# Performance work log

Hardware: AMD Instinct MI355X
Metric: run time of the kernel (lower is better)

Reference implementation:

```python
import jax, jax.numpy as jnp
import numpy as np

HIDDEN = 1152
HEADS = 16
HEAD_DIM = HIDDEN // HEADS  # 72
SCALE = HEAD_DIM ** -0.5


def setup_inputs() -> dict:
    key = jax.random.key(0)
    ks = jax.random.split(key, 9)
    B, S = 16, 729
    init = lambda k, shape: jax.random.normal(k, shape, dtype=jnp.float32) * (shape[0] ** -0.5)
    return {
        "hidden_states": jax.random.normal(ks[0], (B, S, HIDDEN), dtype=jnp.float32),
        "Wq": init(ks[1], (HIDDEN, HIDDEN)), "bq": jnp.zeros((HIDDEN,), jnp.float32),
        "Wk": init(ks[2], (HIDDEN, HIDDEN)), "bk": jnp.zeros((HIDDEN,), jnp.float32),
        "Wv": init(ks[3], (HIDDEN, HIDDEN)), "bv": jnp.zeros((HIDDEN,), jnp.float32),
        "Wo": init(ks[4], (HIDDEN, HIDDEN)), "bo": jnp.zeros((HIDDEN,), jnp.float32),
    }


def reference(hidden_states, Wq, bq, Wk, bk, Wv, bv, Wo, bo):
    B, S, D = hidden_states.shape
    # QKV projections, split heads: [B, S, H, Dh]
    q = (hidden_states @ Wq + bq).reshape(B, S, HEADS, HEAD_DIM)
    k = (hidden_states @ Wk + bk).reshape(B, S, HEADS, HEAD_DIM)
    v = (hidden_states @ Wv + bv).reshape(B, S, HEADS, HEAD_DIM)
    # Scores: [B, H, S, S]
    scores = jnp.einsum("bqhd,bkhd->bhqk", q, k) * jnp.asarray(SCALE, q.dtype)
    # Softmax computed in float32 (as in the original layer), cast back
    attn = jax.nn.softmax(scores.astype(jnp.float32), axis=-1).astype(q.dtype)
    # Weighted values: [B, S, H, Dh] -> [B, S, D]
    out = jnp.einsum("bhqk,bkhd->bqhd", attn, v).reshape(B, S, D)
    return out @ Wo + bo
```

## Files before the change

kernel.cpp:

```cpp
#include <hip/hip_runtime.h>
#include <hip/hip_bf16.h>

#define HD    1152
#define NHD   16
#define DH    72
#define DHP   80
#define NB    16
#define SEQ   729
#define SP    736
#define MTOT  (NB*SEQ)
#define MPAD  11776
#define VROWS 96
#define QSCALE (0.117851130197757930f * 1.4426950408889634f)

typedef __attribute__((ext_vector_type(8))) short short8;
typedef __attribute__((ext_vector_type(4))) float f32x4;
typedef __attribute__((ext_vector_type(16))) float f32x16;
typedef __attribute__((ext_vector_type(4))) unsigned u32x4;
typedef unsigned short us;

__device__ __forceinline__ us f2bf(float x){
  unsigned u = __float_as_uint(x);
  u += 0x7FFFu + ((u >> 16) & 1u);
  return (us)(u >> 16);
}

__device__ __forceinline__ unsigned cvtpk_bf16(float lo, float hi){
  unsigned r;
  asm("v_cvt_pk_bf16_f32 %0, %1, %2" : "=v"(r) : "v"(lo), "v"(hi));
  return r;
}

#define GLD16(g, s) __builtin_amdgcn_global_load_lds( \
    (const __attribute__((address_space(1))) void*)(g), \
    (__attribute__((address_space(3))) void*)(s), 16, 0, 0)

#define OFF_HSB   ((size_t)0)
#define OFF_WQKV  ((size_t)27131904)
#define OFF_WO    ((size_t)35094528)
#define OFF_Q     ((size_t)37748736)
#define OFF_K     ((size_t)67608576)
#define OFF_V     ((size_t)97755136)
#define WS_END    ((size_t)133931008)

#define CVT_BLOCKS 13122
__global__ void prep_kernel(const float* __restrict__ hs, us* __restrict__ hsb,
                            const float* __restrict__ Wq, const float* __restrict__ Wk,
                            const float* __restrict__ Wv, const float* __restrict__ Wo,
                            us* __restrict__ wqkvT, us* __restrict__ woT){
  __shared__ float t[32][33];
  const int b = blockIdx.x, tid = threadIdx.x;
  if (b < CVT_BLOCKS){
    int i = b*256 + tid;
    float4 v = ((const float4*)hs)[i];
    ushort4 o;
    o.x = f2bf(v.x); o.y = f2bf(v.y); o.z = f2bf(v.z); o.w = f2bf(v.w);
    ((ushort4*)hsb)[i] = o;
    return;
  }
  const int bb = b - CVT_BLOCKS;
  const int sel = bb / 1296, cell = bb % 1296;
  const int k0 = (cell/36)*32, n0 = (cell%36)*32;
  const float* W = (sel==0)?Wq:(sel==1)?Wk:(sel==2)?Wv:Wo;
  us* outT = (sel<3) ? (wqkvT + (size_t)sel*HD*HD) : woT;
  const int tx = tid & 31, ty = tid >> 5;
  #pragma unroll
  for (int j=0;j<32;j+=8) t[ty+j][tx] = W[(size_t)(k0+ty+j)*HD + n0 + tx];
  __syncthreads();
  #pragma unroll
  for (int j=0;j<32;j+=8) outT[(size_t)(n0+ty+j)*HD + k0 + tx] = f2bf(t[tx][ty+j]);
}

template<int MODE>
__global__ __launch_bounds__(512, 4) void gemm_kernel(
    const us* __restrict__ A, const us* __restrict__ BT,
    const float* __restrict__ bias_q, const float* __restrict__ bias_k,
    const float* __restrict__ bias_v,
    float* __restrict__ outF,
    us* __restrict__ Qp, us* __restrict__ Kp, us* __restrict__ Vt)
{
  constexpr int TILES_N = (MODE==1) ? 27 : 9;
  constexpr int NPHYS   = (MPAD/128)*TILES_N/2;
  constexpr int NT = HD/32;

  int p;
  {
    int orig = blockIdx.x;
    constexpr int q = NPHYS >> 3, r = NPHYS & 7;
    int xcd = orig & 7, idx = orig >> 3;
    p = (xcd < r ? xcd*(q+1) : r*(q+1) + (xcd-r)*q) + idx;
  }
  const int tid = threadIdx.x, w = tid>>6, l = tid&63;
  const int g  = w>>2;
  const int wl = w&3;
  const int lr = l&15, lg = l>>4;
  const int wm = wl>>1, wn = wl&1;

  const int tile = p*2 + g;
  const int tn = tile % TILES_N, tm = tile / TILES_N;

  __shared__ __align__(16) us As[2][2][4096];
  __shared__ __align__(16) us Bs[2][2][4096];

  const int srow = wl*32 + (l>>2);
  const int scol = (l&3)*8;
  const us* gA = A  + (size_t)(tm*128 + srow)*HD + scol;
  const us* gB = BT + (size_t)(tn*128 + srow)*HD + scol;

#define STAGEP(kb, buf) do { \
    GLD16(gA + (kb),          &As[g][buf][wl*1024]); \
    GLD16(gA + (kb) + 16*HD,  &As[g][buf][wl*1024 + 512]); \
    GLD16(gB + (kb),          &Bs[g][buf][wl*1024]); \
    GLD16(gB + (kb) + 16*HD,  &Bs[g][buf][wl*1024 + 512]); \
  } while(0)

  f32x4 acc[4][4];
  #pragma unroll
  for (int i=0;i<4;i++)
    #pragma unroll
    for (int j=0;j<4;j++) acc[i][j] = (f32x4){0.f,0.f,0.f,0.f};

  STAGEP(0, 0);
  STAGEP(32, 1);

  for (int kt = 0; kt < NT-1; kt++){
    const int cur = kt & 1;
    asm volatile("s_waitcnt vmcnt(4)" ::: "memory");
    __builtin_amdgcn_sched_barrier(0);
    __builtin_amdgcn_s_barrier();
    __builtin_amdgcn_sched_barrier(0);

    short8 af[4], bfr[4];
    #pragma unroll
    for (int mi=0;mi<4;mi++) af[mi]  = *(const short8*)(&As[g][cur][(wm*64 + mi*16 + lr)*32 + lg*8]);
    #pragma unroll
    for (int ni=0;ni<4;ni++) bfr[ni] = *(const short8*)(&Bs[g][cur][(wn*64 + ni*16 + lr)*32 + lg*8]);

    asm volatile("s_waitcnt lgkmcnt(0)" ::: "memory");
    __builtin_amdgcn_sched_barrier(0);
    __builtin_amdgcn_s_barrier();
    __builtin_amdgcn_sched_barrier(0);

    if (kt + 2 < NT) STAGEP((kt+2)*32, cur);

    __builtin_amdgcn_s_setprio(1);
    #pragma unroll
    for (int mi=0;mi<4;mi++)
      #pragma unroll
      for (int ni=0;ni<4;ni++)
        acc[mi][ni] = __builtin_amdgcn_mfma_f32_16x16x32_bf16(af[mi], bfr[ni], acc[mi][ni], 0, 0, 0);
    __builtin_amdgcn_s_setprio(0);
  }
  {
    constexpr int cur = (NT-1) & 1;
    asm volatile("s_waitcnt vmcnt(0)" ::: "memory");
    __builtin_amdgcn_sched_barrier(0);
    __builtin_amdgcn_s_barrier();
    __builtin_amdgcn_sched_barrier(0);
    short8 af[4], bfr[4];
    #pragma unroll
    for (int mi=0;mi<4;mi++) af[mi]  = *(const short8*)(&As[g][cur][(wm*64 + mi*16 + lr)*32 + lg*8]);
    #pragma unroll
    for (int ni=0;ni<4;ni++) bfr[ni] = *(const short8*)(&Bs[g][cur][(wn*64 + ni*16 + lr)*32 + lg*8]);
    #pragma unroll
    for (int mi=0;mi<4;mi++)
      #pragma unroll
      for (int ni=0;ni<4;ni++)
        acc[mi][ni] = __builtin_amdgcn_mfma_f32_16x16x32_bf16(af[mi], bfr[ni], acc[mi][ni], 0, 0, 0);
  }
#undef STAGEP

  if (MODE == 0){
    #pragma unroll
    for (int mi=0;mi<4;mi++){
      #pragma unroll
      for (int j=0;j<4;j++){
        int m = tm*128 + wm*64 + mi*16 + lg*4 + j;
        if (m < MTOT){
          #pragma unroll
          for (int ni=0;ni<4;ni++){
            int n = tn*128 + wn*64 + ni*16 + lr;
            outF[(size_t)m*HD + n] = acc[mi][ni][j] + bias_q[n];
          }
        }
      }
    }
  } else {
    asm volatile("s_waitcnt lgkmcnt(0)" ::: "memory");
    __builtin_amdgcn_sched_barrier(0);
    __builtin_amdgcn_s_barrier();
    __builtin_amdgcn_sched_barrier(0);

    if (tn >= 18){
      float* scr = (float*)(&As[0][0][0]) + w*(16*17);
      #pragma unroll
      for (int mi=0;mi<4;mi++){
        int m = tm*128 + wm*64 + mi*16 + lr;
        int b = m / SEQ;
        int s = m - b*SEQ;
        bool ok = (m < MTOT);
        #pragma unroll
        for (int ni=0;ni<4;ni++){
          #pragma unroll
          for (int j=0;j<4;j++) scr[(lg*4+j)*17 + lr] = acc[mi][ni][j];
          asm volatile("s_waitcnt lgkmcnt(0)" ::: "memory");
          float tv[4];
          #pragma unroll
          for (int j=0;j<4;j++) tv[j] = scr[lr*17 + lg*4 + j];
          asm volatile("s_waitcnt lgkmcnt(0)" ::: "memory");
          if (ok){
            #pragma unroll
            for (int j=0;j<4;j++){
              int n = tn*128 + wn*64 + ni*16 + lg*4 + j;
              int c = n - 2*HD;
              int h = c / DH;
              int d = c - h*DH;
              int bh = b*NHD + h;
              Vt[(size_t)bh*(VROWS*SP) + (size_t)d*SP + s] = f2bf(tv[j] + bias_v[c]);
            }
          }
        }
      }
    } else {
      const bool isQ = (tn < 9);
      const int nbase = isQ ? 0 : HD;
      const float* bias = isQ ? bias_q : bias_k;
      #pragma unroll
      for (int mi=0;mi<4;mi++){
        #pragma unroll
        for (int j=0;j<4;j++){
          int m = tm*128 + wm*64 + mi*16 + lg*4 + j;
          if (m >= MTOT) continue;
          int b = m / SEQ;
          int s = m - b*SEQ;
          #pragma unroll
          for (int ni=0;ni<4;ni++){
            int n = tn*128 + wn*64 + ni*16 + lr;
            int c = n - nbase;
            int h = c / DH;
            int d = c - h*DH;
            int bh = b*NHD + h;
            float v = acc[mi][ni][j] + bias[c];
            if (isQ){
              Qp[(size_t)bh*(SEQ*DHP) + (size_t)s*DHP + d] = f2bf(v*QSCALE);
              if (d < 8)
                Qp[(size_t)bh*(SEQ*DHP) + (size_t)s*DHP + 72 + d] = 0;
            } else {
              Kp[(size_t)bh*(SP*DHP) + (size_t)s*DHP + d] = f2bf(v);
            }
          }
        }
      }
    }
  }
}

__device__ __forceinline__ void pv_subtile(const f32x16 s, const us* __restrict__ vcol,
                                           int hi, f32x16 (&o)[3]){
  unsigned A[4], B[4], xA[4], xB[4];
  #pragma unroll
  for (int g=0; g<4; g++){
    A[g]  = cvtpk_bf16(s[4*g+0], s[4*g+1]);
    B[g]  = cvtpk_bf16(s[4*g+2], s[4*g+3]);
    xA[g] = (unsigned)__shfl_xor((int)A[g], 32);
    xB[g] = (unsigned)__shfl_xor((int)B[g], 32);
  }
  __builtin_amdgcn_s_setprio(1);
  #pragma unroll
  for (int ks=0; ks<2; ks++){
    unsigned w0 = hi ? xA[2*ks+1] : A[2*ks];
    unsigned w1 = hi ? xB[2*ks+1] : B[2*ks];
    unsigned w2 = hi ? A[2*ks+1]  : xA[2*ks];
    unsigned w3 = hi ? B[2*ks+1]  : xB[2*ks];
    u32x4 pw = {w0, w1, w2, w3};
    short8 pa = __builtin_bit_cast(short8, pw);
    #pragma unroll
    for (int dt=0; dt<3; dt++){
      short8 vf = *(const short8*)(vcol + (size_t)(dt*32)*SP + ks*16 + hi*8);
      o[dt] = __builtin_amdgcn_mfma_f32_32x32x16_bf16(pa, vf, o[dt], 0, 0, 0);
    }
  }
  __builtin_amdgcn_s_setprio(0);
}

__global__ __launch_bounds__(256) void attn_kernel(
    const us* __restrict__ Qp, const us* __restrict__ Kp,
    const us* __restrict__ Vt, us* __restrict__ ctx)
{
  const int blk = blockIdx.x;
  const int xcd = blk & 7, ii = blk >> 3;
  const int bh  = xcd*32 + ii/6;
  const int qt6 = ii % 6;
  const int tid = threadIdx.x, w = tid>>6, l = tid&63;
  const int lane = l & 31, hi = l >> 5;

  const int qbase = (qt6*4 + w)*32;
  if (qbase >= SEQ) return;

  const us* Qb = Qp + (size_t)bh*(SEQ*DHP);
  const us* Kb = Kp + (size_t)bh*(SP*DHP);
  const us* Vb = Vt + (size_t)bh*(VROWS*SP);

  int qr = qbase + lane; if (qr > SEQ-1) qr = SEQ-1;
  short8 qf[5];
  #pragma unroll
  for (int c=0;c<5;c++) qf[c] = *(const short8*)(Qb + (size_t)qr*DHP + c*16 + hi*8);

  f32x16 o[3];
  #pragma unroll
  for (int dt=0; dt<3; dt++)
    #pragma unroll
    for (int r=0;r<16;r++) o[dt][r] = 0.f;

  float m = -1e30f, lsum = 0.f;

  for (int kt=0; kt<12; kt++){
    const int kb = kt*64;
    f32x16 s0, s1;
    #pragma unroll
    for (int r=0;r<16;r++){ s0[r]=0.f; s1[r]=0.f; }

    const us* krow0 = Kb + (size_t)(kb + lane)*DHP + hi*8;
    __builtin_amdgcn_s_setprio(1);
    #pragma unroll
    for (int c=0;c<5;c++){
      short8 kf = *(const short8*)(krow0 + c*16);
      s0 = __builtin_amdgcn_mfma_f32_32x32x16_bf16(kf, qf[c], s0, 0, 0, 0);
    }
    __builtin_amdgcn_s_setprio(0);
    if (kt < 11){
      const us* krow1 = krow0 + 32*DHP;
      __builtin_amdgcn_s_setprio(1);
      #pragma unroll
      for (int c=0;c<5;c++){
        short8 kf = *(const short8*)(krow1 + c*16);
        s1 = __builtin_amdgcn_mfma_f32_32x32x16_bf16(kf, qf[c], s1, 0, 0, 0);
      }
      __builtin_amdgcn_s_setprio(0);
    } else {
      #pragma unroll
      for (int r=0;r<16;r++){
        const int base = 704 + (r&3) + 8*(r>>2);
        s0[r] = (base + 4*hi >= SEQ) ? -1e30f : s0[r];
        s1[r] = -1e30f;
      }
    }

    float tmax = -1e30f;
    #pragma unroll
    for (int r=0;r<16;r++) tmax = fmaxf(tmax, fmaxf(s0[r], s1[r]));
    tmax = fmaxf(tmax, __shfl_xor(tmax, 32));

    if (!__all(tmax <= m + 8.0f)){
      float mn = fmaxf(m, tmax);
      float sc = exp2f(m - mn);
      m = mn;
      lsum *= sc;
      #pragma unroll
      for (int dt=0; dt<3; dt++)
        #pragma unroll
        for (int r=0;r<16;r++) o[dt][r] *= sc;
    }

    float su = 0.f;
    #pragma unroll
    for (int r=0;r<16;r++){ float pp = exp2f(s0[r]-m); s0[r]=pp; su += pp; }
    #pragma unroll
    for (int r=0;r<16;r++){ float pp = exp2f(s1[r]-m); s1[r]=pp; su += pp; }
    su += __shfl_xor(su, 32);
    lsum += su;

    const us* vcol = Vb + (size_t)lane*SP + kb;
    pv_subtile(s0, vcol, hi, o);
    if (kt < 11) pv_subtile(s1, vcol + 32, hi, o);
  }

  float linv = 1.0f / lsum;
  const int b = bh >> 4, h = bh & 15;
  #pragma unroll
  for (int r=0;r<16;r++){
    const int qloc = (r&3) + 8*(r>>2) + 4*hi;
    float lv = __shfl(linv, qloc);
    int q = qbase + qloc;
    if (q < SEQ){
      us* crow = ctx + ((size_t)(b*SEQ + q))*HD + h*DH;
      #pragma unroll
      for (int dt=0; dt<3; dt++){
        int d = dt*32 + lane;
        if (d < DH) crow[d] = f2bf(o[dt][r] * lv);
      }
    }
  }
}

extern "C" void kernel_launch(void* const* d_in, const int* in_sizes, int n_in,
                              void* d_out, int out_size, void* d_ws, size_t ws_size,
                              hipStream_t stream) {
  const float* hs = (const float*)d_in[0];
  const float* Wq = (const float*)d_in[1]; const float* bq = (const float*)d_in[2];
  const float* Wk = (const float*)d_in[3]; const float* bk = (const float*)d_in[4];
  const float* Wv = (const float*)d_in[5]; const float* bv = (const float*)d_in[6];
  const float* Wo = (const float*)d_in[7]; const float* bo = (const float*)d_in[8];
  float* out = (float*)d_out;
  char* ws = (char*)d_ws;
  if (ws_size < WS_END) return;

  us* hsb   = (us*)(ws + OFF_HSB);
  us* wqkvT = (us*)(ws + OFF_WQKV);
  us* woT   = (us*)(ws + OFF_WO);
  us* Qp    = (us*)(ws + OFF_Q);
  us* Kp    = (us*)(ws + OFF_K);
  us* Vt    = (us*)(ws + OFF_V);
  us* ctx   = hsb;

  prep_kernel<<<CVT_BLOCKS + 4*1296, 256, 0, stream>>>(hs, hsb, Wq, Wk, Wv, Wo,
                                                       wqkvT, woT);

  gemm_kernel<1><<<(MPAD/128)*27/2, 512, 0, stream>>>(hsb, wqkvT, bq, bk, bv,
                                                      nullptr, Qp, Kp, Vt);

  attn_kernel<<<1536, 256, 0, stream>>>(Qp, Kp, Vt, ctx);

  gemm_kernel<0><<<(MPAD/128)*9/2, 512, 0, stream>>>(ctx, woT, bo, nullptr, nullptr,
                                                     out, nullptr, nullptr, nullptr);
}
```

Measured before the change: 345.9 us.

## Process two 32-row query subtiles per wave to reuse K/V loads

Each wave in the attention kernel now handles 64 query rows as two 32-row subtiles, and blocks shrink from 256 to 128 threads. K and V fragment addresses are shared across both subtiles, so each loaded K/V tile feeds twice as much MFMA work. The online softmax state is duplicated per subtile. This roughly doubles accumulator and Q-fragment register use, which may lower occupancy. Query tiles past SEQ are no longer skipped early and are handled by clamping rows and masking the stores.

```diff
diff --git a/kernel.cpp b/kernel.cpp
--- a/kernel.cpp
+++ b/kernel.cpp
@@ -283,7 +283,7 @@
   __builtin_amdgcn_s_setprio(0);
 }
 
-__global__ __launch_bounds__(256) void attn_kernel(
+__global__ __launch_bounds__(128) void attn_kernel(
     const us* __restrict__ Qp, const us* __restrict__ Kp,
     const us* __restrict__ Vt, us* __restrict__ ctx)
 {
@@ -294,100 +294,111 @@
   const int tid = threadIdx.x, w = tid>>6, l = tid&63;
   const int lane = l & 31, hi = l >> 5;
 
-  const int qbase = (qt6*4 + w)*32;
-  if (qbase >= SEQ) return;
+  const int qbase = (qt6*2 + w)*64;
 
   const us* Qb = Qp + (size_t)bh*(SEQ*DHP);
   const us* Kb = Kp + (size_t)bh*(SP*DHP);
   const us* Vb = Vt + (size_t)bh*(VROWS*SP);
 
-  int qr = qbase + lane; if (qr > SEQ-1) qr = SEQ-1;
-  short8 qf[5];
-  #pragma unroll
-  for (int c=0;c<5;c++) qf[c] = *(const short8*)(Qb + (size_t)qr*DHP + c*16 + hi*8);
-
-  f32x16 o[3];
-  #pragma unroll
-  for (int dt=0; dt<3; dt++)
-    #pragma unroll
-    for (int r=0;r<16;r++) o[dt][r] = 0.f;
-
-  float m = -1e30f, lsum = 0.f;
+  short8 qf[2][5];
+  #pragma unroll
+  for (int st=0; st<2; st++){
+    int qr = qbase + st*32 + lane; if (qr > SEQ-1) qr = SEQ-1;
+    #pragma unroll
+    for (int c=0;c<5;c++) qf[st][c] = *(const short8*)(Qb + (size_t)qr*DHP + c*16 + hi*8);
+  }
+
+  f32x16 o[2][3];
+  #pragma unroll
+  for (int st=0; st<2; st++)
+    #pragma unroll
+    for (int dt=0; dt<3; dt++)
+      #pragma unroll
+      for (int r=0;r<16;r++) o[st][dt][r] = 0.f;
+
+  float m[2] = {-1e30f,-1e30f}, lsum[2] = {0.f,0.f};
 
   for (int kt=0; kt<12; kt++){
     const int kb = kt*64;
-    f32x16 s0, s1;
-    #pragma unroll
-    for (int r=0;r<16;r++){ s0[r]=0.f; s1[r]=0.f; }
-
     const us* krow0 = Kb + (size_t)(kb + lane)*DHP + hi*8;
-    __builtin_amdgcn_s_setprio(1);
-    #pragma unroll
-    for (int c=0;c<5;c++){
-      short8 kf = *(const short8*)(krow0 + c*16);
-      s0 = __builtin_amdgcn_mfma_f32_32x32x16_bf16(kf, qf[c], s0, 0, 0, 0);
+    const us* vcol  = Vb + (size_t)lane*SP + kb;
+
+    #pragma unroll
+    for (int st=0; st<2; st++){
+      f32x16 s0, s1;
+      #pragma unroll
+      for (int r=0;r<16;r++){ s0[r]=0.f; s1[r]=0.f; }
+
+      __builtin_amdgcn_s_setprio(1);
+      #pragma unroll
+      for (int c=0;c<5;c++){
+        short8 kf = *(const short8*)(krow0 + c*16);
+        s0 = __builtin_amdgcn_mfma_f32_32x32x16_bf16(kf, qf[st][c], s0, 0, 0, 0);
+      }
+      __builtin_amdgcn_s_setprio(0);
+      if (kt < 11){
+        const us* krow1 = krow0 + 32*DHP;
+        __builtin_amdgcn_s_setprio(1);
+        #pragma unroll
+        for (int c=0;c<5;c++){
+          short8 kf = *(const short8*)(krow1 + c*16);
+          s1 = __builtin_amdgcn_mfma_f32_32x32x16_bf16(kf, qf[st][c], s1, 0, 0, 0);
+        }
+        __builtin_amdgcn_s_setprio(0);
+      } else {
+        #pragma unroll
+        for (int r=0;r<16;r++){
+          const int base = 704 + (r&3) + 8*(r>>2);
+          s0[r] = (base + 4*hi >= SEQ) ? -1e30f : s0[r];
+          s1[r] = -1e30f;
+        }
+      }
+
+      float tmax = -1e30f;
+      #pragma unroll
+      for (int r=0;r<16;r++) tmax = fmaxf(tmax, fmaxf(s0[r], s1[r]));
+      tmax = fmaxf(tmax, __shfl_xor(tmax, 32));
+
+      if (!__all(tmax <= m[st] + 8.0f)){
+        float mn = fmaxf(m[st], tmax);
+        float sc = exp2f(m[st] - mn);
+        m[st] = mn;
+        lsum[st] *= sc;
+        #pragma unroll
+        for (int dt=0; dt<3; dt++)
+          #pragma unroll
+          for (int r=0;r<16;r++) o[st][dt][r] *= sc;
+      }
+
+      float su = 0.f;
+      #pragma unroll
+      for (int r=0;r<16;r++){ float pp = exp2f(s0[r]-m[st]); s0[r]=pp; su += pp; }
+      #pragma unroll
+      for (int r=0;r<16;r++){ float pp = exp2f(s1[r]-m[st]); s1[r]=pp; su += pp; }
+      su += __shfl_xor(su, 32);
+      lsum[st] += su;
+
+      pv_subtile(s0, vcol, hi, o[st]);
+      if (kt < 11) pv_subtile(s1, vcol + 32, hi, o[st]);
     }
-    __builtin_amdgcn_s_setprio(0);
-    if (kt < 11){
-      const us* krow1 = krow0 + 32*DHP;
-      __builtin_amdgcn_s_setprio(1);
-      #pragma unroll
-      for (int c=0;c<5;c++){
-        short8 kf = *(const short8*)(krow1 + c*16);
-        s1 = __builtin_amdgcn_mfma_f32_32x32x16_bf16(kf, qf[c], s1, 0, 0, 0);
-      }
-      __builtin_amdgcn_s_setprio(0);
-    } else {
-      #pragma unroll
-      for (int r=0;r<16;r++){
-        const int base = 704 + (r&3) + 8*(r>>2);
-        s0[r] = (base + 4*hi >= SEQ) ? -1e30f : s0[r];
-        s1[r] = -1e30f;
-      }
-    }
-
-    float tmax = -1e30f;
-    #pragma unroll
-    for (int r=0;r<16;r++) tmax = fmaxf(tmax, fmaxf(s0[r], s1[r]));
-    tmax = fmaxf(tmax, __shfl_xor(tmax, 32));
-
-    if (!__all(tmax <= m + 8.0f)){
-      float mn = fmaxf(m, tmax);
-      float sc = exp2f(m - mn);
-      m = mn;
-      lsum *= sc;
-      #pragma unroll
-      for (int dt=0; dt<3; dt++)
-        #pragma unroll
-        for (int r=0;r<16;r++) o[dt][r] *= sc;
-    }
-
-    float su = 0.f;
-    #pragma unroll
-    for (int r=0;r<16;r++){ float pp = exp2f(s0[r]-m); s0[r]=pp; su += pp; }
-    #pragma unroll
-    for (int r=0;r<16;r++){ float pp = exp2f(s1[r]-m); s1[r]=pp; su += pp; }
-    su += __shfl_xor(su, 32);
-    lsum += su;
-
-    const us* vcol = Vb + (size_t)lane*SP + kb;
-    pv_subtile(s0, vcol, hi, o);
-    if (kt < 11) pv_subtile(s1, vcol + 32, hi, o);
-  }
-
-  float linv = 1.0f / lsum;
+  }
+
   const int b = bh >> 4, h = bh & 15;
   #pragma unroll
-  for (int r=0;r<16;r++){
-    const int qloc = (r&3) + 8*(r>>2) + 4*hi;
-    float lv = __shfl(linv, qloc);
-    int q = qbase + qloc;
-    if (q < SEQ){
-      us* crow = ctx + ((size_t)(b*SEQ + q))*HD + h*DH;
-      #pragma unroll
-      for (int dt=0; dt<3; dt++){
-        int d = dt*32 + lane;
-        if (d < DH) crow[d] = f2bf(o[dt][r] * lv);
+  for (int st=0; st<2; st++){
+    float linv = 1.0f / lsum[st];
+    #pragma unroll
+    for (int r=0;r<16;r++){
+      const int qloc = (r&3) + 8*(r>>2) + 4*hi;
+      float lv = __shfl(linv, qloc);
+      int q = qbase + st*32 + qloc;
+      if (q < SEQ){
+        us* crow = ctx + ((size_t)(b*SEQ + q))*HD + h*DH;
+        #pragma unroll
+        for (int dt=0; dt<3; dt++){
+          int d = dt*32 + lane;
+          if (d < DH) crow[d] = f2bf(o[st][dt][r] * lv);
+        }
       }
     }
   }
@@ -419,7 +430,7 @@
   gemm_kernel<1><<<(MPAD/128)*27/2, 512, 0, stream>>>(hsb, wqkvT, bq, bk, bv,
                                                       nullptr, Qp, Kp, Vt);
 
-  attn_kernel<<<1536, 256, 0, stream>>>(Qp, Kp, Vt, ctx);
+  attn_kernel<<<1536, 128, 0, stream>>>(Qp, Kp, Vt, ctx);
 
   gemm_kernel<0><<<(MPAD/128)*9/2, 512, 0, stream>>>(ctx, woT, bo, nullptr, nullptr,
                                                      out, nullptr, nullptr, nullptr);
```

Result: slower. 404.8 us (+17.0%).
